# Kernel optimization log

Hardware: AMD Instinct MI355X
Metric: run time of the kernel (lower is better)

The kernel has to match this reference:

```python
import jax, jax.numpy as jnp
import numpy as np


def setup_inputs() -> dict:
    key = jax.random.key(0)
    kx, kq, kk, kv = jax.random.split(key, 4)
    B, S, D_IN, H, D_OUT = 2, 2048, 768, 12, 64
    scale = 0.02
    return {
        "x": jax.random.normal(kx, (B, S, D_IN), dtype=jnp.float32),
        "Wq": jax.random.normal(kq, (H, D_IN, D_OUT), dtype=jnp.float32) * scale,
        "Wk": jax.random.normal(kk, (H, D_IN, D_OUT), dtype=jnp.float32) * scale,
        "Wv": jax.random.normal(kv, (H, D_IN, D_OUT), dtype=jnp.float32) * scale,
    }


def reference(x, Wq, Wk, Wv):
    # x: [B, S, d_in]; Wq/Wk/Wv: [H, d_in, d_out] (stacked per-head Linear weights, no bias)
    B, S, _ = x.shape
    H, _, d_out = Wq.shape
    q = jnp.einsum("bsd,hde->bhse", x, Wq)  # [B, H, S, d_out]
    k = jnp.einsum("bsd,hde->bhse", x, Wk)
    v = jnp.einsum("bsd,hde->bhse", x, Wv)
    scores = jnp.einsum("bhse,bhte->bhst", q, k) / jnp.sqrt(jnp.float32(d_out))
    causal = jnp.tril(jnp.ones((S, S), dtype=bool))  # True = keep
    scores = jnp.where(causal, scores, jnp.float32(-jnp.inf))
    attn = jax.nn.softmax(scores, axis=-1)  # dropout = 0.0 -> identity
    ctx = jnp.einsum("bhst,bhte->bhse", attn, v)  # [B, H, S, d_out]
    # concat heads along last dim: [B, S, H*d_out]
    return ctx.transpose(0, 2, 1, 3).reshape(B, S, H * d_out)
```

## Files before the change

### kernel.cpp

```cpp
#include <hip/hip_runtime.h>
#include <hip/hip_bf16.h>


typedef short bf16x8 __attribute__((ext_vector_type(8)));
typedef short bf16x4 __attribute__((ext_vector_type(4)));
typedef float f32x4  __attribute__((ext_vector_type(4)));

#define MFMA16(a, b, c)  __builtin_amdgcn_mfma_f32_16x16x32_bf16((a), (b), (c), 0, 0, 0)
#define MFMAK16(a, b, c) __builtin_amdgcn_mfma_f32_16x16x16bf16_1k((a), (b), (c), 0, 0, 0)

static __device__ __forceinline__ unsigned short f2bf(float f) {
    unsigned int u = __builtin_bit_cast(unsigned int, f);
    u += 0x7fffu + ((u >> 16) & 1u);
    return (unsigned short)(u >> 16);
}

static __device__ __forceinline__ int sw(int row, int cb) {
    return (row << 7) + (cb ^ ((row & 7) << 4));
}

static __device__ __forceinline__ void gld16(const void* g, void* l) {
    __builtin_amdgcn_global_load_lds(
        (__attribute__((address_space(1))) void*)g,
        (__attribute__((address_space(3))) void*)l, 16, 0, 0);
}

__global__ __launch_bounds__(256) void prep_x(const float* __restrict__ x,
                                              char* __restrict__ xb) {
    const int stile = blockIdx.x, ks = blockIdx.y;
    const int t = threadIdx.x;
    const int row = t >> 2, k16 = (t & 3) * 16;
    const float* src = x + (size_t)(stile * 64 + row) * 768 + ks * 64 + k16;
    char* img = xb + ((size_t)stile * 12 + ks) * 8192;
    const float4 v0 = *(const float4*)(src);
    const float4 v1 = *(const float4*)(src + 4);
    const float4 v2 = *(const float4*)(src + 8);
    const float4 v3 = *(const float4*)(src + 12);
    bf16x8 o0, o1;
    o0[0] = (short)f2bf(v0.x); o0[1] = (short)f2bf(v0.y);
    o0[2] = (short)f2bf(v0.z); o0[3] = (short)f2bf(v0.w);
    o0[4] = (short)f2bf(v1.x); o0[5] = (short)f2bf(v1.y);
    o0[6] = (short)f2bf(v1.z); o0[7] = (short)f2bf(v1.w);
    o1[0] = (short)f2bf(v2.x); o1[1] = (short)f2bf(v2.y);
    o1[2] = (short)f2bf(v2.z); o1[3] = (short)f2bf(v2.w);
    o1[4] = (short)f2bf(v3.x); o1[5] = (short)f2bf(v3.y);
    o1[6] = (short)f2bf(v3.z); o1[7] = (short)f2bf(v3.w);
    *(bf16x8*)(img + sw(row, k16 * 2)) = o0;
    *(bf16x8*)(img + sw(row, k16 * 2 + 16)) = o1;
}

__global__ __launch_bounds__(256) void prep_wt(const float* __restrict__ Wq,
                                               const float* __restrict__ Wk,
                                               const float* __restrict__ Wv,
                                               char* __restrict__ wtb) {
    __shared__ float tile[64][65];
    const int w = blockIdx.x / 12, h = blockIdx.x % 12;
    const int dt = blockIdx.y;
    const float* W = (w == 0) ? Wq : (w == 1) ? Wk : Wv;
    const int t = threadIdx.x;
    for (int i = 0; i < 4; ++i) {
        int c = t + i * 256;
        int d = c >> 4, e4 = (c & 15) * 4;
        const float4 v = *(const float4*)(W + (size_t)(h * 768 + dt * 64 + d) * 64 + e4);
        tile[d][e4 + 0] = v.x; tile[d][e4 + 1] = v.y;
        tile[d][e4 + 2] = v.z; tile[d][e4 + 3] = v.w;
    }
    __syncthreads();
    char* img = wtb + ((size_t)((w * 12 + h) * 12) + dt) * 8192;
    for (int i = 0; i < 4; ++i) {
        int c = t + i * 256;
        int e = c >> 4, d4 = (c & 15) * 4;
        ushort4 o;
        o.x = f2bf(tile[d4 + 0][e]); o.y = f2bf(tile[d4 + 1][e]);
        o.z = f2bf(tile[d4 + 2][e]); o.w = f2bf(tile[d4 + 3][e]);
        *(ushort4*)(img + e * 128 + ((d4 * 2) ^ ((e & 7) << 4))) = o;
    }
}

__global__ __launch_bounds__(256) void proj_qkv(const char* __restrict__ xb,
                                                const char* __restrict__ wtb,
                                                unsigned short* __restrict__ q,
                                                unsigned short* __restrict__ ksw,
                                                char* __restrict__ vsw) {
    __shared__ __align__(16) char smem[65536];
    const int stile = blockIdx.x;
    const int h = blockIdx.y;
    const int t = threadIdx.x;
    const int wave = t >> 6, lane = t & 63;
    const int lhi = lane >> 4, llo = lane & 15;
    const int wr = wave >> 1, wc = wave & 1;

    const char* asrc = xb + (size_t)stile * 12 * 8192;

    f32x4 acc[3][2][2] = {};

    #define STAGE(KS, BUF)                                                       \
        do {                                                                     \
            const char* s0 = asrc + (KS) * 8192;                                 \
            char* d0 = smem + (BUF) * 32768;                                     \
            gld16(s0 + t * 16, d0 + t * 16);                                     \
            gld16(s0 + t * 16 + 4096, d0 + t * 16 + 4096);                       \
            for (int w3 = 0; w3 < 3; ++w3) {                                     \
                const char* s1 = wtb + ((size_t)((w3 * 12 + h) * 12) + (KS)) * 8192; \
                char* d1 = smem + (BUF) * 32768 + (1 + w3) * 8192;               \
                gld16(s1 + t * 16, d1 + t * 16);                                 \
                gld16(s1 + t * 16 + 4096, d1 + t * 16 + 4096);                   \
            }                                                                    \
        } while (0)

    STAGE(0, 0);
    __syncthreads();
    int cur = 0;
    for (int ks = 0; ks < 12; ++ks) {
        if (ks < 11) STAGE(ks + 1, cur ^ 1);
        char* Alds = smem + cur * 32768;
        #pragma unroll
        for (int kk = 0; kk < 2; ++kk) {
            bf16x8 a[2];
            #pragma unroll
            for (int m = 0; m < 2; ++m)
                a[m] = *(const bf16x8*)(Alds + sw(wr * 32 + m * 16 + llo, kk * 64 + lhi * 16));
            #pragma unroll
            for (int w3 = 0; w3 < 3; ++w3) {
                char* Blds = Alds + (1 + w3) * 8192;
                #pragma unroll
                for (int n = 0; n < 2; ++n) {
                    bf16x8 b = *(const bf16x8*)(Blds + sw(wc * 32 + n * 16 + llo, kk * 64 + lhi * 16));
                    #pragma unroll
                    for (int m = 0; m < 2; ++m)
                        acc[w3][m][n] = MFMA16(a[m], b, acc[w3][m][n]);
                }
            }
        }
        __syncthreads();
        cur ^= 1;
    }
    #undef STAGE

    const float SCALE_Q = 0.18033688011112042f;
    const int bglob = stile >> 5, ktile = stile & 31;
    const int bh = bglob * 12 + h;
    #pragma unroll
    for (int m = 0; m < 2; ++m)
        for (int n = 0; n < 2; ++n)
            for (int r = 0; r < 4; ++r) {
                int s = (stile * 64 + wr * 32 + m * 16 + lhi * 4 + r) & 2047;
                int e = wc * 32 + n * 16 + llo;
                q[(size_t)(bh * 2048 + s) * 64 + e] = f2bf(acc[0][m][n][r] * SCALE_Q);
            }
    unsigned short* kdst = ksw + ((size_t)bh * 32 + ktile) * 4096;
    #pragma unroll
    for (int m = 0; m < 2; ++m)
        for (int n = 0; n < 2; ++n)
            for (int r = 0; r < 4; ++r) {
                int kk = wr * 32 + m * 16 + lhi * 4 + r;
                int e = wc * 32 + n * 16 + llo;
                kdst[kk * 64 + (e ^ ((kk & 7) << 3))] = f2bf(acc[1][m][n][r]);
            }
    char* vtimg = smem;
    __syncthreads();
    #pragma unroll
    for (int m = 0; m < 2; ++m)
        for (int n = 0; n < 2; ++n)
            for (int r = 0; r < 4; ++r) {
                int kk = wr * 32 + m * 16 + lhi * 4 + r;
                int e = wc * 32 + n * 16 + llo;
                int pos = (((kk >> 2) & 3) * 32 + (kk >> 4) * 8 + (kk & 3) * 2) ^ ((e & 7) << 4);
                *(unsigned short*)(vtimg + e * 128 + pos) = f2bf(acc[2][m][n][r]);
            }
    __syncthreads();
    {
        char* dst = vsw + ((size_t)bh * 32 + ktile) * 8192;
        #pragma unroll
        for (int i = 0; i < 2; ++i)
            *(float4*)(dst + t * 16 + i * 4096) =
                *(const float4*)(vtimg + t * 16 + i * 4096);
    }
}

__global__ __launch_bounds__(256) void attn(const unsigned short* __restrict__ Q,
                                            const char* __restrict__ Ksw,
                                            const char* __restrict__ Vsw,
                                            float* __restrict__ out) {
    __shared__ __align__(16) char smem[32768];
    const int t = threadIdx.x, wave = t >> 6, lane = t & 63;
    const int lhi = lane >> 4, llo = lane & 15;
    const int bid = blockIdx.x;
    const int bh = bid % 24;
    const int qt = 31 - bid / 24;
    const unsigned short* Qg = Q + (size_t)bh * 2048 * 64;
    const char* Kg = Ksw + (size_t)bh * 32 * 8192;
    const char* Vg = Vsw + (size_t)bh * 32 * 8192;

    const int q0 = qt * 64 + wave * 16;
    bf16x8 qa[2];
    #pragma unroll
    for (int kk = 0; kk < 2; ++kk)
        qa[kk] = *(const bf16x8*)(Qg + (size_t)(q0 + llo) * 64 + kk * 32 + lhi * 8);

    f32x4 acc[4] = {};
    float m_r = -1e30f, l_r = 0.f;

    #define ASTAGE(KT, BUF)                                              \
        do {                                                             \
            const char* ks_ = Kg + (size_t)(KT) * 8192;                  \
            const char* vs_ = Vg + (size_t)(KT) * 8192;                  \
            char* kd = smem + (BUF) * 8192;                              \
            char* vd = smem + 16384 + (BUF) * 8192;                      \
            gld16(ks_ + t * 16, kd + t * 16);                            \
            gld16(ks_ + t * 16 + 4096, kd + t * 16 + 4096);              \
            gld16(vs_ + t * 16, vd + t * 16);                            \
            gld16(vs_ + t * 16 + 4096, vd + t * 16 + 4096);              \
        } while (0)

    ASTAGE(0, 0);
    __syncthreads();
    int cur = 0;
    for (int kt = 0; kt <= qt; ++kt) {
        if (kt < qt) ASTAGE(kt + 1, cur ^ 1);
        char* Kb = smem + cur * 8192;
        char* Vb = smem + 16384 + cur * 8192;

        f32x4 sc[4];
        __builtin_amdgcn_s_setprio(1);
        #pragma unroll
        for (int n = 0; n < 4; ++n) {
            f32x4 z = {};
            #pragma unroll
            for (int kk = 0; kk < 2; ++kk) {
                bf16x8 bk = *(const bf16x8*)(Kb + sw(n * 16 + llo, kk * 64 + lhi * 16));
                z = MFMA16(bk, qa[kk], z);
            }
            sc[n] = z;
        }
        __builtin_amdgcn_s_setprio(0);
        if (kt == qt) {
            #pragma unroll
            for (int n = 0; n < 4; ++n)
                #pragma unroll
                for (int r = 0; r < 4; ++r)
                    if (kt * 64 + n * 16 + lhi * 4 + r > q0 + llo) sc[n][r] = -1e30f;
        }
        float pmax = fmaxf(
            fmaxf(fmaxf(fmaxf(sc[0][0], sc[0][1]), fmaxf(sc[0][2], sc[0][3])),
                  fmaxf(fmaxf(sc[1][0], sc[1][1]), fmaxf(sc[1][2], sc[1][3]))),
            fmaxf(fmaxf(fmaxf(sc[2][0], sc[2][1]), fmaxf(sc[2][2], sc[2][3])),
                  fmaxf(fmaxf(sc[3][0], sc[3][1]), fmaxf(sc[3][2], sc[3][3]))));
        if (__any(pmax > m_r + 8.0f)) {
            float tm = fmaxf(pmax, __shfl_xor(pmax, 16, 64));
            tm = fmaxf(tm, __shfl_xor(tm, 32, 64));
            float nm = fmaxf(m_r, tm);
            float corr = exp2f(m_r - nm);
            m_r = nm;
            l_r *= corr;
            #pragma unroll
            for (int n = 0; n < 4; ++n)
                #pragma unroll
                for (int r = 0; r < 4; ++r) acc[n][r] *= corr;
        }
        bf16x4 pf[4];
        float ps = 0.f;
        #pragma unroll
        for (int kb = 0; kb < 4; ++kb) {
            float p0 = exp2f(sc[kb][0] - m_r), p1 = exp2f(sc[kb][1] - m_r);
            float p2 = exp2f(sc[kb][2] - m_r), p3 = exp2f(sc[kb][3] - m_r);
            ps += (p0 + p1) + (p2 + p3);
            unsigned int w0, w1;
            asm("v_cvt_pk_bf16_f32 %0, %1, %2" : "=v"(w0) : "v"(p0), "v"(p1));
            asm("v_cvt_pk_bf16_f32 %0, %1, %2" : "=v"(w1) : "v"(p2), "v"(p3));
            unsigned long long u = ((unsigned long long)w1 << 32) | w0;
            pf[kb] = __builtin_bit_cast(bf16x4, u);
        }
        l_r += ps;
        __builtin_amdgcn_s_setprio(1);
        #pragma unroll
        for (int n = 0; n < 4; ++n) {
            const int row = n * 16 + llo;
            bf16x8 v8a = *(const bf16x8*)(Vb + sw(row, lhi * 32));
            bf16x8 v8b = *(const bf16x8*)(Vb + sw(row, lhi * 32 + 16));
            f32x4 a = acc[n];
            a = MFMAK16(__builtin_shufflevector(v8a, v8a, 0, 1, 2, 3), pf[0], a);
            a = MFMAK16(__builtin_shufflevector(v8a, v8a, 4, 5, 6, 7), pf[1], a);
            a = MFMAK16(__builtin_shufflevector(v8b, v8b, 0, 1, 2, 3), pf[2], a);
            a = MFMAK16(__builtin_shufflevector(v8b, v8b, 4, 5, 6, 7), pf[3], a);
            acc[n] = a;
        }
        __builtin_amdgcn_s_setprio(0);
        __syncthreads();
        cur ^= 1;
    }
    #undef ASTAGE
    l_r += __shfl_xor(l_r, 16, 64);
    l_r += __shfl_xor(l_r, 32, 64);
    const float inv = 1.0f / l_r;
    const int b = bh / 12, h = bh - b * 12;
    #pragma unroll
    for (int n = 0; n < 4; ++n) {
        float4 o;
        o.x = acc[n][0] * inv; o.y = acc[n][1] * inv;
        o.z = acc[n][2] * inv; o.w = acc[n][3] * inv;
        *(float4*)(out + (size_t)(b * 2048 + q0 + llo) * 768 + h * 64 + n * 16 + lhi * 4) = o;
    }
}

extern "C" void kernel_launch(void* const* d_in, const int* in_sizes, int n_in,
                              void* d_out, int out_size, void* d_ws, size_t ws_size,
                              hipStream_t stream) {
    const float* x  = (const float*)d_in[0];
    const float* Wq = (const float*)d_in[1];
    const float* Wk = (const float*)d_in[2];
    const float* Wv = (const float*)d_in[3];
    float* out = (float*)d_out;

    char* ws = (char*)d_ws;
    char*           wtb = ws;
    unsigned short* q   = (unsigned short*)(ws + 3538944);
    unsigned short* ksw = (unsigned short*)(ws + 9830400);
    char*           vsw = (char*)(ws + 16121856);
    char*           xb  = (char*)(ws + 22413312);

    hipLaunchKernelGGL(prep_x, dim3(64, 12), dim3(256), 0, stream, x, xb);
    hipLaunchKernelGGL(prep_wt, dim3(36, 12), dim3(256), 0, stream, Wq, Wk, Wv, wtb);
    hipLaunchKernelGGL(proj_qkv, dim3(64, 12), dim3(256), 0, stream,
                       xb, wtb, q, ksw, vsw);
    hipLaunchKernelGGL(attn, dim3(768), dim3(256), 0, stream, q, (const char*)ksw, vsw, out);
}
```

Baseline: 76.93 us.

## Pair causal query strips per block and merge prep kernels into one launch

Result: slower. 81.97 us (+6.5%).

```diff
diff --git a/kernel.cpp b/kernel.cpp
--- a/kernel.cpp
+++ b/kernel.cpp
@@ -25,55 +25,57 @@
         (__attribute__((address_space(3))) void*)l, 16, 0, 0);
 }
 
-__global__ __launch_bounds__(256) void prep_x(const float* __restrict__ x,
-                                              char* __restrict__ xb) {
-    const int stile = blockIdx.x, ks = blockIdx.y;
+__global__ __launch_bounds__(256) void prep(const float* __restrict__ x,
+                                            const float* __restrict__ Wq,
+                                            const float* __restrict__ Wk,
+                                            const float* __restrict__ Wv,
+                                            char* __restrict__ xb,
+                                            char* __restrict__ wtb) {
+    __shared__ float tile[64][65];
+    const int bid = blockIdx.x;
     const int t = threadIdx.x;
-    const int row = t >> 2, k16 = (t & 3) * 16;
-    const float* src = x + (size_t)(stile * 64 + row) * 768 + ks * 64 + k16;
-    char* img = xb + ((size_t)stile * 12 + ks) * 8192;
-    const float4 v0 = *(const float4*)(src);
-    const float4 v1 = *(const float4*)(src + 4);
-    const float4 v2 = *(const float4*)(src + 8);
-    const float4 v3 = *(const float4*)(src + 12);
-    bf16x8 o0, o1;
-    o0[0] = (short)f2bf(v0.x); o0[1] = (short)f2bf(v0.y);
-    o0[2] = (short)f2bf(v0.z); o0[3] = (short)f2bf(v0.w);
-    o0[4] = (short)f2bf(v1.x); o0[5] = (short)f2bf(v1.y);
-    o0[6] = (short)f2bf(v1.z); o0[7] = (short)f2bf(v1.w);
-    o1[0] = (short)f2bf(v2.x); o1[1] = (short)f2bf(v2.y);
-    o1[2] = (short)f2bf(v2.z); o1[3] = (short)f2bf(v2.w);
-    o1[4] = (short)f2bf(v3.x); o1[5] = (short)f2bf(v3.y);
-    o1[6] = (short)f2bf(v3.z); o1[7] = (short)f2bf(v3.w);
-    *(bf16x8*)(img + sw(row, k16 * 2)) = o0;
-    *(bf16x8*)(img + sw(row, k16 * 2 + 16)) = o1;
-}
-
-__global__ __launch_bounds__(256) void prep_wt(const float* __restrict__ Wq,
-                                               const float* __restrict__ Wk,
-                                               const float* __restrict__ Wv,
-                                               char* __restrict__ wtb) {
-    __shared__ float tile[64][65];
-    const int w = blockIdx.x / 12, h = blockIdx.x % 12;
-    const int dt = blockIdx.y;
-    const float* W = (w == 0) ? Wq : (w == 1) ? Wk : Wv;
-    const int t = threadIdx.x;
-    for (int i = 0; i < 4; ++i) {
-        int c = t + i * 256;
-        int d = c >> 4, e4 = (c & 15) * 4;
-        const float4 v = *(const float4*)(W + (size_t)(h * 768 + dt * 64 + d) * 64 + e4);
-        tile[d][e4 + 0] = v.x; tile[d][e4 + 1] = v.y;
-        tile[d][e4 + 2] = v.z; tile[d][e4 + 3] = v.w;
-    }
-    __syncthreads();
-    char* img = wtb + ((size_t)((w * 12 + h) * 12) + dt) * 8192;
-    for (int i = 0; i < 4; ++i) {
-        int c = t + i * 256;
-        int e = c >> 4, d4 = (c & 15) * 4;
-        ushort4 o;
-        o.x = f2bf(tile[d4 + 0][e]); o.y = f2bf(tile[d4 + 1][e]);
-        o.z = f2bf(tile[d4 + 2][e]); o.w = f2bf(tile[d4 + 3][e]);
-        *(ushort4*)(img + e * 128 + ((d4 * 2) ^ ((e & 7) << 4))) = o;
+    if (bid < 768) {
+        const int stile = bid & 63, ks = bid >> 6;
+        const int row = t >> 2, k16 = (t & 3) * 16;
+        const float* src = x + (size_t)(stile * 64 + row) * 768 + ks * 64 + k16;
+        char* img = xb + ((size_t)stile * 12 + ks) * 8192;
+        const float4 v0 = *(const float4*)(src);
+        const float4 v1 = *(const float4*)(src + 4);
+        const float4 v2 = *(const float4*)(src + 8);
+        const float4 v3 = *(const float4*)(src + 12);
+        bf16x8 o0, o1;
+        o0[0] = (short)f2bf(v0.x); o0[1] = (short)f2bf(v0.y);
+        o0[2] = (short)f2bf(v0.z); o0[3] = (short)f2bf(v0.w);
+        o0[4] = (short)f2bf(v1.x); o0[5] = (short)f2bf(v1.y);
+        o0[6] = (short)f2bf(v1.z); o0[7] = (short)f2bf(v1.w);
+        o1[0] = (short)f2bf(v2.x); o1[1] = (short)f2bf(v2.y);
+        o1[2] = (short)f2bf(v2.z); o1[3] = (short)f2bf(v2.w);
+        o1[4] = (short)f2bf(v3.x); o1[5] = (short)f2bf(v3.y);
+        o1[6] = (short)f2bf(v3.z); o1[7] = (short)f2bf(v3.w);
+        *(bf16x8*)(img + sw(row, k16 * 2)) = o0;
+        *(bf16x8*)(img + sw(row, k16 * 2 + 16)) = o1;
+    } else {
+        const int idx = bid - 768;
+        const int wh = idx % 36, dt = idx / 36;
+        const int w = wh / 12, h = wh % 12;
+        const float* W = (w == 0) ? Wq : (w == 1) ? Wk : Wv;
+        for (int i = 0; i < 4; ++i) {
+            int c = t + i * 256;
+            int d = c >> 4, e4 = (c & 15) * 4;
+            const float4 v = *(const float4*)(W + (size_t)(h * 768 + dt * 64 + d) * 64 + e4);
+            tile[d][e4 + 0] = v.x; tile[d][e4 + 1] = v.y;
+            tile[d][e4 + 2] = v.z; tile[d][e4 + 3] = v.w;
+        }
+        __syncthreads();
+        char* img = wtb + ((size_t)(wh * 12) + dt) * 8192;
+        for (int i = 0; i < 4; ++i) {
+            int c = t + i * 256;
+            int e = c >> 4, d4 = (c & 15) * 4;
+            ushort4 o;
+            o.x = f2bf(tile[d4 + 0][e]); o.y = f2bf(tile[d4 + 1][e]);
+            o.z = f2bf(tile[d4 + 2][e]); o.w = f2bf(tile[d4 + 3][e]);
+            *(ushort4*)(img + e * 128 + ((d4 * 2) ^ ((e & 7) << 4))) = o;
+        }
     }
 }
 
@@ -178,7 +180,7 @@
     }
 }
 
-__global__ __launch_bounds__(256) void attn(const unsigned short* __restrict__ Q,
+__global__ __launch_bounds__(128) void attn(const unsigned short* __restrict__ Q,
                                             const char* __restrict__ Ksw,
                                             const char* __restrict__ Vsw,
                                             float* __restrict__ out) {
@@ -187,19 +189,27 @@
     const int lhi = lane >> 4, llo = lane & 15;
     const int bid = blockIdx.x;
     const int bh = bid % 24;
-    const int qt = 31 - bid / 24;
+    const int p = bid / 24;
+    const int sA = p, sB = 63 - p;
+    const int kaA = sA >> 1;
+    const int kaB = sB >> 1;
     const unsigned short* Qg = Q + (size_t)bh * 2048 * 64;
     const char* Kg = Ksw + (size_t)bh * 32 * 8192;
     const char* Vg = Vsw + (size_t)bh * 32 * 8192;
-
-    const int q0 = qt * 64 + wave * 16;
-    bf16x8 qa[2];
-    #pragma unroll
-    for (int kk = 0; kk < 2; ++kk)
-        qa[kk] = *(const bf16x8*)(Qg + (size_t)(q0 + llo) * 64 + kk * 32 + lhi * 8);
+    const int b = bh / 12, h = bh - b * 12;
+
+    const int q0A = sA * 32 + wave * 16, q0B = sB * 32 + wave * 16;
+    bf16x8 qaA[2], qaB[2];
+    #pragma unroll
+    for (int kk = 0; kk < 2; ++kk) {
+        qaA[kk] = *(const bf16x8*)(Qg + (size_t)(q0A + llo) * 64 + kk * 32 + lhi * 8);
+        qaB[kk] = *(const bf16x8*)(Qg + (size_t)(q0B + llo) * 64 + kk * 32 + lhi * 8);
+    }
 
     f32x4 acc[4] = {};
     float m_r = -1e30f, l_r = 0.f;
+    bf16x8 qa[2]; qa[0] = qaA[0]; qa[1] = qaA[1];
+    int q0 = q0A, ktmax = kaA, kt = 0;
 
     #define ASTAGE(KT, BUF)                                              \
         do {                                                             \
@@ -207,17 +217,23 @@
             const char* vs_ = Vg + (size_t)(KT) * 8192;                  \
             char* kd = smem + (BUF) * 8192;                              \
             char* vd = smem + 16384 + (BUF) * 8192;                      \
-            gld16(ks_ + t * 16, kd + t * 16);                            \
-            gld16(ks_ + t * 16 + 4096, kd + t * 16 + 4096);              \
-            gld16(vs_ + t * 16, vd + t * 16);                            \
-            gld16(vs_ + t * 16 + 4096, vd + t * 16 + 4096);              \
+            _Pragma("unroll")                                            \
+            for (int i = 0; i < 4; ++i) {                                \
+                gld16(ks_ + t * 16 + i * 2048, kd + t * 16 + i * 2048);  \
+                gld16(vs_ + t * 16 + i * 2048, vd + t * 16 + i * 2048);  \
+            }                                                            \
         } while (0)
 
     ASTAGE(0, 0);
     __syncthreads();
     int cur = 0;
-    for (int kt = 0; kt <= qt; ++kt) {
-        if (kt < qt) ASTAGE(kt + 1, cur ^ 1);
+    const int nIter = kaA + kaB + 2;
+    for (int g = 0; g < nIter; ++g) {
+        if (g + 1 < nIter) {
+            int ng = g + 1;
+            int nkt = (ng <= kaA) ? ng : ng - kaA - 1;
+            ASTAGE(nkt, cur ^ 1);
+        }
         char* Kb = smem + cur * 8192;
         char* Vb = smem + 16384 + cur * 8192;
 
@@ -234,7 +250,7 @@
             sc[n] = z;
         }
         __builtin_amdgcn_s_setprio(0);
-        if (kt == qt) {
+        if (kt == ktmax) {
             #pragma unroll
             for (int n = 0; n < 4; ++n)
                 #pragma unroll
@@ -288,12 +304,34 @@
         __builtin_amdgcn_s_setprio(0);
         __syncthreads();
         cur ^= 1;
+
+        if (g == kaA) {
+            float lr = l_r;
+            lr += __shfl_xor(lr, 16, 64);
+            lr += __shfl_xor(lr, 32, 64);
+            float inv = 1.0f / lr;
+            #pragma unroll
+            for (int n = 0; n < 4; ++n) {
+                float4 o;
+                o.x = acc[n][0] * inv; o.y = acc[n][1] * inv;
+                o.z = acc[n][2] * inv; o.w = acc[n][3] * inv;
+                *(float4*)(out + (size_t)(b * 2048 + q0 + llo) * 768 + h * 64 + n * 16 + lhi * 4) = o;
+            }
+            #pragma unroll
+            for (int n = 0; n < 4; ++n)
+                #pragma unroll
+                for (int r = 0; r < 4; ++r) acc[n][r] = 0.f;
+            m_r = -1e30f; l_r = 0.f;
+            qa[0] = qaB[0]; qa[1] = qaB[1];
+            q0 = q0B; ktmax = kaB; kt = 0;
+        } else {
+            ++kt;
+        }
     }
     #undef ASTAGE
     l_r += __shfl_xor(l_r, 16, 64);
     l_r += __shfl_xor(l_r, 32, 64);
     const float inv = 1.0f / l_r;
-    const int b = bh / 12, h = bh - b * 12;
     #pragma unroll
     for (int n = 0; n < 4; ++n) {
         float4 o;
@@ -319,9 +357,8 @@
     char*           vsw = (char*)(ws + 16121856);
     char*           xb  = (char*)(ws + 22413312);
 
-    hipLaunchKernelGGL(prep_x, dim3(64, 12), dim3(256), 0, stream, x, xb);
-    hipLaunchKernelGGL(prep_wt, dim3(36, 12), dim3(256), 0, stream, Wq, Wk, Wv, wtb);
+    hipLaunchKernelGGL(prep, dim3(1200), dim3(256), 0, stream, x, Wq, Wk, Wv, xb, wtb);
     hipLaunchKernelGGL(proj_qkv, dim3(64, 12), dim3(256), 0, stream,
                        xb, wtb, q, ksw, vsw);
-    hipLaunchKernelGGL(attn, dim3(768), dim3(256), 0, stream, q, (const char*)ksw, vsw, out);
-}
+    hipLaunchKernelGGL(attn, dim3(768), dim3(128), 0, stream, q, (const char*)ksw, vsw, out);
+}
```
